# Kernel tuning notes

Hardware: AMD Instinct MI355X
Metric: run time of the kernel (lower is better)

## Reference

```python
import jax, jax.numpy as jnp
import numpy as np

NUM_EXPERTS = 8
HIDDEN = 2048
INTER = 1408
TOKENS = 2048
TOP_K = 2


def setup_inputs() -> dict:
    key = jax.random.key(0)
    k1, k2, k3, k4, k5, k6 = jax.random.split(key, 6)
    hidden_states = jax.random.normal(k1, (TOKENS, HIDDEN), dtype=jnp.float32)
    top_k_index = jax.random.randint(k2, (TOKENS, TOP_K), 0, NUM_EXPERTS)
    top_k_weights = jax.random.uniform(k3, (TOKENS, TOP_K), dtype=jnp.float32)
    top_k_weights = top_k_weights / top_k_weights.sum(-1, keepdims=True)  # router-normalized
    scale = 0.02
    Wg = jax.random.normal(k4, (NUM_EXPERTS, INTER, HIDDEN), dtype=jnp.float32) * scale
    Wu = jax.random.normal(k5, (NUM_EXPERTS, INTER, HIDDEN), dtype=jnp.float32) * scale
    Wd = jax.random.normal(k6, (NUM_EXPERTS, HIDDEN, INTER), dtype=jnp.float32) * scale
    return {
        "hidden_states": hidden_states,
        "top_k_index": top_k_index,
        "top_k_weights": top_k_weights,
        "Wg": Wg,
        "Wu": Wu,
        "Wd": Wd,
    }


def reference(hidden_states, top_k_index, top_k_weights, Wg, Wu, Wd):
    # Combine weight per (token, expert): sum over top-k slots routed to that
    # expert (index_add in the original accumulates duplicate routes identically).
    E = Wg.shape[0]
    cw = (jax.nn.one_hot(top_k_index, E, dtype=hidden_states.dtype)
          * top_k_weights[..., None]).sum(axis=1)            # [T, E]
    # Per-expert SwiGLU MLP computed as grouped GEMMs over all tokens.
    gate = jnp.einsum('th,eih->tei', hidden_states, Wg)       # [T, E, I]
    up = jnp.einsum('th,eih->tei', hidden_states, Wu)         # [T, E, I]
    h = jax.nn.silu(gate) * up                                # [T, E, I]
    out_e = jnp.einsum('tei,ehi->teh', h, Wd)                 # [T, E, H]
    # Weighted combine: tokens not routed to an expert have cw == 0.
    return jnp.einsum('teh,te->th', out_e, cw)                # [T, H]
```

## Files before the change

### kernel.cpp

```cpp
#include <hip/hip_runtime.h>
#include <hip/hip_bf16.h>
#include <stdint.h>

#define TOKENS 2048
#define HIDDEN 2048
#define INTER  1408
#define NEXP   8
#define NPAIR  4096

typedef __attribute__((ext_vector_type(8))) short bf16x8;
typedef __attribute__((ext_vector_type(4))) float f32x4;

static __device__ __forceinline__ unsigned short f2b(float f) {
    union { float f; uint32_t u; } v; v.f = f;
    uint32_t r = (v.u + 0x7FFFu + ((v.u >> 16) & 1u)) >> 16;
    return (unsigned short)r;
}

static __device__ __forceinline__ uint32_t cvtpk(float lo, float hi) {
    uint32_t r;
    asm("v_cvt_pk_bf16_f32 %0, %1, %2" : "=v"(r) : "v"(lo), "v"(hi));
    return r;
}

#define GLDS(SRC, DST) \
    __builtin_amdgcn_global_load_lds( \
        (const __attribute__((address_space(1))) unsigned int*)(SRC), \
        (__attribute__((address_space(3))) unsigned int*)(DST), 16, 0, 0)

__global__ void route_k(const int* __restrict__ idx,
                        int* __restrict__ off, int* __restrict__ tok,
                        int* __restrict__ inv) {
    __shared__ int cnt[NEXP];
    __shared__ int cur[NEXP];
    int tid = threadIdx.x;
    if (tid < NEXP) cnt[tid] = 0;
    __syncthreads();
    for (int i = tid; i < NPAIR; i += 256) atomicAdd(&cnt[idx[i]], 1);
    __syncthreads();
    if (tid == 0) {
        int s = 0;
        for (int e = 0; e < NEXP; ++e) { off[e] = s; cur[e] = s; s += cnt[e]; }
        off[NEXP] = s;
    }
    __syncthreads();
    for (int i = tid; i < NPAIR; i += 256) {
        int e = idx[i];
        int p = atomicAdd(&cur[e], 1);
        tok[p] = i >> 1;
        inv[i] = p;
    }
}

__global__ void conv_k(const float* __restrict__ x, unsigned short* __restrict__ xb, int n) {
    int i = (blockIdx.x * blockDim.x + threadIdx.x) * 4;
    if (i < n) {
        float4 v = *(const float4*)(x + i);
        ushort4 o;
        o.x = f2b(v.x); o.y = f2b(v.y); o.z = f2b(v.z); o.w = f2b(v.w);
        *(ushort4*)(xb + i) = o;
    }
}

__global__ void combine_k(const float* __restrict__ tmp, const int* __restrict__ inv,
                          const float* __restrict__ tw, float* __restrict__ out) {
    int i = blockIdx.x * blockDim.x + threadIdx.x;
    int t = i >> 9;
    int c = (i & 511) * 4;
    int p0 = inv[2 * t], p1 = inv[2 * t + 1];
    float w0 = tw[2 * t], w1 = tw[2 * t + 1];
    float4 x = *(const float4*)(tmp + (size_t)p0 * HIDDEN + c);
    float4 y = *(const float4*)(tmp + (size_t)p1 * HIDDEN + c);
    float4 o;
    o.x = w0 * x.x + w1 * y.x;
    o.y = w0 * x.y + w1 * y.y;
    o.z = w0 * x.z + w1 * y.z;
    o.w = w0 * x.w + w1 * y.w;
    *(float4*)(out + (size_t)t * HIDDEN + c) = o;
}


__global__ __launch_bounds__(256, 4) void gemm1_k(
    const unsigned short* __restrict__ Xb,
    const float* __restrict__ Wg, const float* __restrict__ Wu,
    const int* __restrict__ off, const int* __restrict__ tok,
    unsigned short* __restrict__ H) {

    const int e    = blockIdx.z;
    const int o0   = off[e];
    const int cnt  = off[e + 1] - o0;
    const int row0 = blockIdx.y * 128;
    if (row0 >= cnt) return;
    const int col0 = blockIdx.x * 64;

    __shared__ __align__(16) unsigned short sA[2][128 * 32];
    __shared__ __align__(16) unsigned short sG[2][64 * 32];
    __shared__ __align__(16) unsigned short sU[2][64 * 32];
    __shared__ int stok[128];

    const int tid = threadIdx.x;
    if (tid < 128) {
        int r = row0 + tid;
        stok[tid] = tok[o0 + (r < cnt ? r : cnt - 1)];
    }
    __syncthreads();

    int sa_[2]; const unsigned short* gA[2];
    #pragma unroll
    for (int j = 0; j < 2; ++j) {
        int s = tid + 256 * j, r = s >> 2, q = s & 3;
        sa_[j] = s * 8;
        gA[j] = Xb + (size_t)stok[r] * HIDDEN + ((q ^ ((r >> 1) & 3)) << 3);
    }
    int sb_; const float* fG; const float* fU;
    {
        int s = tid, r = s >> 2, q = s & 3;
        sb_ = s * 8;
        int c = (q ^ ((r >> 1) & 3)) << 3;
        fG = Wg + ((size_t)e * INTER + col0 + r) * HIDDEN + c;
        fU = Wu + ((size_t)e * INTER + col0 + r) * HIDDEN + c;
    }

    const int wave = tid >> 6, lane = tid & 63;
    const int wm = (wave >> 1) * 64, wn = (wave & 1) * 32;
    const int lm = lane & 15, quad = lane >> 4;
    const int swz = ((quad ^ ((lane >> 1) & 3)) << 3);

    f32x4 accg[4][2], accu[4][2];
    #pragma unroll
    for (int i = 0; i < 4; ++i)
        #pragma unroll
        for (int j = 0; j < 2; ++j) {
            accg[i][j] = (f32x4){0.f, 0.f, 0.f, 0.f};
            accu[i][j] = (f32x4){0.f, 0.f, 0.f, 0.f};
        }

    GLDS(gA[0], &sA[0][sa_[0]]);
    GLDS(gA[1], &sA[0][sa_[1]]);
    {
        float4 g0 = *(const float4*)(fG);
        float4 g1 = *(const float4*)(fG + 4);
        float4 u0 = *(const float4*)(fU);
        float4 u1 = *(const float4*)(fU + 4);
        *(int4*)&sG[0][sb_] = make_int4(cvtpk(g0.x, g0.y), cvtpk(g0.z, g0.w),
                                        cvtpk(g1.x, g1.y), cvtpk(g1.z, g1.w));
        *(int4*)&sU[0][sb_] = make_int4(cvtpk(u0.x, u0.y), cvtpk(u0.z, u0.w),
                                        cvtpk(u1.x, u1.y), cvtpk(u1.z, u1.w));
    }
    __syncthreads();

    const int NS = HIDDEN / 32;
    for (int ks = 0; ks < NS; ++ks) {
        const int b = ks & 1;
        float4 g0, g1, u0, u1;
        if (ks + 1 < NS) {
            const int ko = (ks + 1) * 32;
            GLDS(gA[0] + ko, &sA[b ^ 1][sa_[0]]);
            GLDS(gA[1] + ko, &sA[b ^ 1][sa_[1]]);
            g0 = *(const float4*)(fG + ko);
            g1 = *(const float4*)(fG + ko + 4);
            u0 = *(const float4*)(fU + ko);
            u1 = *(const float4*)(fU + ko + 4);
        }
        bf16x8 af[4], gf[2], uf[2];
        #pragma unroll
        for (int mi = 0; mi < 4; ++mi)
            af[mi] = *(const bf16x8*)&sA[b][(wm + mi * 16 + lm) * 32 + swz];
        #pragma unroll
        for (int ni = 0; ni < 2; ++ni) {
            gf[ni] = *(const bf16x8*)&sG[b][(wn + ni * 16 + lm) * 32 + swz];
            uf[ni] = *(const bf16x8*)&sU[b][(wn + ni * 16 + lm) * 32 + swz];
        }
        #pragma unroll
        for (int mi = 0; mi < 4; ++mi)
            #pragma unroll
            for (int ni = 0; ni < 2; ++ni) {
                accg[mi][ni] = __builtin_amdgcn_mfma_f32_16x16x32_bf16(af[mi], gf[ni], accg[mi][ni], 0, 0, 0);
                accu[mi][ni] = __builtin_amdgcn_mfma_f32_16x16x32_bf16(af[mi], uf[ni], accu[mi][ni], 0, 0, 0);
            }
        if (ks + 1 < NS) {
            *(int4*)&sG[b ^ 1][sb_] = make_int4(cvtpk(g0.x, g0.y), cvtpk(g0.z, g0.w),
                                                cvtpk(g1.x, g1.y), cvtpk(g1.z, g1.w));
            *(int4*)&sU[b ^ 1][sb_] = make_int4(cvtpk(u0.x, u0.y), cvtpk(u0.z, u0.w),
                                                cvtpk(u1.x, u1.y), cvtpk(u1.z, u1.w));
        }
        __syncthreads();
    }

    #pragma unroll
    for (int mi = 0; mi < 4; ++mi) {
        #pragma unroll
        for (int reg = 0; reg < 4; ++reg) {
            int lr = wm + mi * 16 + quad * 4 + reg;
            int r  = row0 + lr;
            if (r < cnt) {
                size_t hrow = (size_t)(o0 + r) * INTER;
                #pragma unroll
                for (int ni = 0; ni < 2; ++ni) {
                    float g = accg[mi][ni][reg];
                    float u = accu[mi][ni][reg];
                    float h = g / (1.f + __expf(-g)) * u;
                    H[hrow + col0 + wn + ni * 16 + lm] = f2b(h);
                }
            }
        }
    }
}

__global__ __launch_bounds__(256, 4) void gemm2_k(
    const unsigned short* __restrict__ H,
    const float* __restrict__ Wd,
    const int* __restrict__ off,
    float* __restrict__ tmp) {

    const int e    = blockIdx.z;
    const int o0   = off[e];
    const int cnt  = off[e + 1] - o0;
    const int row0 = blockIdx.y * 128;
    if (row0 >= cnt) return;
    const int col0 = blockIdx.x * 64;

    __shared__ __align__(16) unsigned short sA[2][128 * 32];
    __shared__ __align__(16) unsigned short sB[2][64 * 32];

    const int tid = threadIdx.x;

    int sa_[2]; const unsigned short* gA[2];
    #pragma unroll
    for (int j = 0; j < 2; ++j) {
        int s = tid + 256 * j, r = s >> 2, q = s & 3;
        sa_[j] = s * 8;
        int c = (q ^ ((r >> 1) & 3)) << 3;
        int gr = row0 + r; if (gr >= cnt) gr = cnt - 1;
        gA[j] = H + (size_t)(o0 + gr) * INTER + c;
    }
    int sb_; const float* fB;
    {
        int s = tid, r = s >> 2, q = s & 3;
        sb_ = s * 8;
        int c = (q ^ ((r >> 1) & 3)) << 3;
        fB = Wd + ((size_t)e * HIDDEN + col0 + r) * INTER + c;
    }

    const int wave = tid >> 6, lane = tid & 63;
    const int wm = (wave >> 1) * 64, wn = (wave & 1) * 32;
    const int lm = lane & 15, quad = lane >> 4;
    const int swz = ((quad ^ ((lane >> 1) & 3)) << 3);

    f32x4 acc[4][2];
    #pragma unroll
    for (int i = 0; i < 4; ++i)
        #pragma unroll
        for (int j = 0; j < 2; ++j) acc[i][j] = (f32x4){0.f, 0.f, 0.f, 0.f};

    GLDS(gA[0], &sA[0][sa_[0]]);
    GLDS(gA[1], &sA[0][sa_[1]]);
    {
        float4 b0 = *(const float4*)(fB);
        float4 b1 = *(const float4*)(fB + 4);
        *(int4*)&sB[0][sb_] = make_int4(cvtpk(b0.x, b0.y), cvtpk(b0.z, b0.w),
                                        cvtpk(b1.x, b1.y), cvtpk(b1.z, b1.w));
    }
    __syncthreads();

    const int NS = INTER / 32;
    for (int ks = 0; ks < NS; ++ks) {
        const int b = ks & 1;
        float4 b0, b1;
        if (ks + 1 < NS) {
            const int ko = (ks + 1) * 32;
            GLDS(gA[0] + ko, &sA[b ^ 1][sa_[0]]);
            GLDS(gA[1] + ko, &sA[b ^ 1][sa_[1]]);
            b0 = *(const float4*)(fB + ko);
            b1 = *(const float4*)(fB + ko + 4);
        }
        bf16x8 af[4], bf[2];
        #pragma unroll
        for (int mi = 0; mi < 4; ++mi)
            af[mi] = *(const bf16x8*)&sA[b][(wm + mi * 16 + lm) * 32 + swz];
        #pragma unroll
        for (int ni = 0; ni < 2; ++ni)
            bf[ni] = *(const bf16x8*)&sB[b][(wn + ni * 16 + lm) * 32 + swz];
        #pragma unroll
        for (int mi = 0; mi < 4; ++mi)
            #pragma unroll
            for (int ni = 0; ni < 2; ++ni)
                acc[mi][ni] = __builtin_amdgcn_mfma_f32_16x16x32_bf16(af[mi], bf[ni], acc[mi][ni], 0, 0, 0);
        if (ks + 1 < NS) {
            *(int4*)&sB[b ^ 1][sb_] = make_int4(cvtpk(b0.x, b0.y), cvtpk(b0.z, b0.w),
                                                cvtpk(b1.x, b1.y), cvtpk(b1.z, b1.w));
        }
        __syncthreads();
    }

    #pragma unroll
    for (int mi = 0; mi < 4; ++mi) {
        #pragma unroll
        for (int reg = 0; reg < 4; ++reg) {
            int lr = wm + mi * 16 + quad * 4 + reg;
            int r  = row0 + lr;
            if (r < cnt) {
                size_t trow = (size_t)(o0 + r) * HIDDEN;
                #pragma unroll
                for (int ni = 0; ni < 2; ++ni)
                    tmp[trow + col0 + wn + ni * 16 + lm] = acc[mi][ni][reg];
            }
        }
    }
}

extern "C" void kernel_launch(void* const* d_in, const int* in_sizes, int n_in,
                              void* d_out, int out_size, void* d_ws, size_t ws_size,
                              hipStream_t stream) {
    const float* X   = (const float*)d_in[0];
    const int*   idx = (const int*)d_in[1];
    const float* tw  = (const float*)d_in[2];
    const float* Wg  = (const float*)d_in[3];
    const float* Wu  = (const float*)d_in[4];
    const float* Wd  = (const float*)d_in[5];
    float* out = (float*)d_out;

    char* ws = (char*)d_ws;
    const size_t OFF_TOK = 64;
    const size_t OFF_INV = OFF_TOK + (size_t)NPAIR * 4;
    const size_t OFF_XB  = 65536;
    const size_t OFF_H   = OFF_XB + (size_t)TOKENS * HIDDEN * 2;
    const size_t OFF_TMP = OFF_H + (size_t)NPAIR * INTER * 2;

    int*            off = (int*)ws;
    int*            tok = (int*)(ws + OFF_TOK);
    int*            inv = (int*)(ws + OFF_INV);
    unsigned short* Xb  = (unsigned short*)(ws + OFF_XB);
    unsigned short* H   = (unsigned short*)(ws + OFF_H);
    float*          tmp = (float*)(ws + OFF_TMP);

    route_k<<<1, 256, 0, stream>>>(idx, off, tok, inv);
    conv_k<<<(TOKENS * HIDDEN / 4 + 255) / 256, 256, 0, stream>>>(X, Xb, TOKENS * HIDDEN);

    gemm1_k<<<dim3(INTER / 64, NPAIR / 128, NEXP), 256, 0, stream>>>(Xb, Wg, Wu, off, tok, H);
    gemm2_k<<<dim3(HIDDEN / 64, NPAIR / 128, NEXP), 256, 0, stream>>>(H, Wd, off, tmp);
    combine_k<<<TOKENS * (HIDDEN / 4) / 256, 256, 0, stream>>>(tmp, inv, tw, out);
}
```

Measured before the change: 433.8 us.

## Deepen weight prefetch with register double-buffering and manual vmcnt waits

Both expert GEMM main loops are unrolled by two. The fp32 weight tiles are now loaded two K-steps ahead into alternating register sets, instead of one step ahead. `__syncthreads` is replaced by explicit `s_waitcnt vmcnt(N)` plus `s_barrier`, so the look-ahead weight loads can stay in flight across the barrier while the async A-tile loads to LDS are still guaranteed complete. Scheduling fences keep the compiler from reordering the loads. The aim is to hide global-memory latency on the weight stream, at the cost of extra registers and fragile hand-counted waitcnt values.

```diff
diff --git a/kernel.cpp b/kernel.cpp
--- a/kernel.cpp
+++ b/kernel.cpp
@@ -27,6 +27,10 @@
     __builtin_amdgcn_global_load_lds( \
         (const __attribute__((address_space(1))) unsigned int*)(SRC), \
         (__attribute__((address_space(3))) unsigned int*)(DST), 16, 0, 0)
+
+#define WAITVM(N) asm volatile("s_waitcnt vmcnt(" #N ") lgkmcnt(0)" ::: "memory")
+#define BARRIER() asm volatile("s_barrier" ::: "memory")
+#define SCHED_FENCE() __builtin_amdgcn_sched_barrier(0)
 
 __global__ void route_k(const int* __restrict__ idx,
                         int* __restrict__ off, int* __restrict__ tok,
@@ -80,6 +84,9 @@
 }
 
 
+struct W4 { float4 g0, g1, u0, u1; };
+struct W2 { float4 b0, b1; };
+
 __global__ __launch_bounds__(256, 4) void gemm1_k(
     const unsigned short* __restrict__ Xb,
     const float* __restrict__ Wg, const float* __restrict__ Wu,
@@ -135,8 +142,11 @@
             accu[i][j] = (f32x4){0.f, 0.f, 0.f, 0.f};
         }
 
+    const int NS = HIDDEN / 32;
+
     GLDS(gA[0], &sA[0][sa_[0]]);
     GLDS(gA[1], &sA[0][sa_[1]]);
+    SCHED_FENCE();
     {
         float4 g0 = *(const float4*)(fG);
         float4 g1 = *(const float4*)(fG + 4);
@@ -147,45 +157,63 @@
         *(int4*)&sU[0][sb_] = make_int4(cvtpk(u0.x, u0.y), cvtpk(u0.z, u0.w),
                                         cvtpk(u1.x, u1.y), cvtpk(u1.z, u1.w));
     }
-    __syncthreads();
-
-    const int NS = HIDDEN / 32;
-    for (int ks = 0; ks < NS; ++ks) {
-        const int b = ks & 1;
-        float4 g0, g1, u0, u1;
-        if (ks + 1 < NS) {
-            const int ko = (ks + 1) * 32;
-            GLDS(gA[0] + ko, &sA[b ^ 1][sa_[0]]);
-            GLDS(gA[1] + ko, &sA[b ^ 1][sa_[1]]);
-            g0 = *(const float4*)(fG + ko);
-            g1 = *(const float4*)(fG + ko + 4);
-            u0 = *(const float4*)(fU + ko);
-            u1 = *(const float4*)(fU + ko + 4);
-        }
-        bf16x8 af[4], gf[2], uf[2];
-        #pragma unroll
-        for (int mi = 0; mi < 4; ++mi)
-            af[mi] = *(const bf16x8*)&sA[b][(wm + mi * 16 + lm) * 32 + swz];
-        #pragma unroll
-        for (int ni = 0; ni < 2; ++ni) {
-            gf[ni] = *(const bf16x8*)&sG[b][(wn + ni * 16 + lm) * 32 + swz];
-            uf[ni] = *(const bf16x8*)&sU[b][(wn + ni * 16 + lm) * 32 + swz];
-        }
-        #pragma unroll
-        for (int mi = 0; mi < 4; ++mi)
-            #pragma unroll
-            for (int ni = 0; ni < 2; ++ni) {
-                accg[mi][ni] = __builtin_amdgcn_mfma_f32_16x16x32_bf16(af[mi], gf[ni], accg[mi][ni], 0, 0, 0);
-                accu[mi][ni] = __builtin_amdgcn_mfma_f32_16x16x32_bf16(af[mi], uf[ni], accu[mi][ni], 0, 0, 0);
-            }
-        if (ks + 1 < NS) {
-            *(int4*)&sG[b ^ 1][sb_] = make_int4(cvtpk(g0.x, g0.y), cvtpk(g0.z, g0.w),
-                                                cvtpk(g1.x, g1.y), cvtpk(g1.z, g1.w));
-            *(int4*)&sU[b ^ 1][sb_] = make_int4(cvtpk(u0.x, u0.y), cvtpk(u0.z, u0.w),
-                                                cvtpk(u1.x, u1.y), cvtpk(u1.z, u1.w));
-        }
-        __syncthreads();
-    }
+    W4 wA, wB;
+    wA.g0 = *(const float4*)(fG + 32);
+    wA.g1 = *(const float4*)(fG + 36);
+    wA.u0 = *(const float4*)(fU + 32);
+    wA.u1 = *(const float4*)(fU + 36);
+    SCHED_FENCE();
+    asm volatile("s_waitcnt lgkmcnt(0)" ::: "memory");
+    BARRIER();
+
+#define G1_STEP(KS, WCUR, WNEXT)                                               \
+    {                                                                          \
+        const int b = (KS) & 1;                                                \
+        if ((KS) + 1 < NS) {                                                   \
+            const int ko = ((KS) + 1) * 32;                                    \
+            GLDS(gA[0] + ko, &sA[b ^ 1][sa_[0]]);                              \
+            GLDS(gA[1] + ko, &sA[b ^ 1][sa_[1]]);                              \
+        }                                                                      \
+        SCHED_FENCE();                                                         \
+        if ((KS) + 2 < NS) {                                                   \
+            const int ko2 = ((KS) + 2) * 32;                                   \
+            WNEXT.g0 = *(const float4*)(fG + ko2);                             \
+            WNEXT.g1 = *(const float4*)(fG + ko2 + 4);                         \
+            WNEXT.u0 = *(const float4*)(fU + ko2);                             \
+            WNEXT.u1 = *(const float4*)(fU + ko2 + 4);                         \
+        }                                                                      \
+        SCHED_FENCE();                                                         \
+        bf16x8 af[4], gf[2], uf[2];                                            \
+        _Pragma("unroll")                                                      \
+        for (int mi = 0; mi < 4; ++mi)                                         \
+            af[mi] = *(const bf16x8*)&sA[b][(wm + mi * 16 + lm) * 32 + swz];   \
+        _Pragma("unroll")                                                      \
+        for (int ni = 0; ni < 2; ++ni) {                                       \
+            gf[ni] = *(const bf16x8*)&sG[b][(wn + ni * 16 + lm) * 32 + swz];   \
+            uf[ni] = *(const bf16x8*)&sU[b][(wn + ni * 16 + lm) * 32 + swz];   \
+        }                                                                      \
+        _Pragma("unroll")                                                      \
+        for (int mi = 0; mi < 4; ++mi)                                         \
+            _Pragma("unroll")                                                  \
+            for (int ni = 0; ni < 2; ++ni) {                                   \
+                accg[mi][ni] = __builtin_amdgcn_mfma_f32_16x16x32_bf16(af[mi], gf[ni], accg[mi][ni], 0, 0, 0); \
+                accu[mi][ni] = __builtin_amdgcn_mfma_f32_16x16x32_bf16(af[mi], uf[ni], accu[mi][ni], 0, 0, 0); \
+            }                                                                  \
+        if ((KS) + 1 < NS) {                                                   \
+            *(int4*)&sG[b ^ 1][sb_] = make_int4(cvtpk(WCUR.g0.x, WCUR.g0.y), cvtpk(WCUR.g0.z, WCUR.g0.w), \
+                                                cvtpk(WCUR.g1.x, WCUR.g1.y), cvtpk(WCUR.g1.z, WCUR.g1.w)); \
+            *(int4*)&sU[b ^ 1][sb_] = make_int4(cvtpk(WCUR.u0.x, WCUR.u0.y), cvtpk(WCUR.u0.z, WCUR.u0.w), \
+                                                cvtpk(WCUR.u1.x, WCUR.u1.y), cvtpk(WCUR.u1.z, WCUR.u1.w)); \
+        }                                                                      \
+        if ((KS) + 2 < NS) { WAITVM(4); } else { WAITVM(0); }                  \
+        BARRIER();                                                             \
+    }
+
+    for (int ks = 0; ks < NS; ks += 2) {
+        G1_STEP(ks,     wA, wB);
+        G1_STEP(ks + 1, wB, wA);
+    }
+#undef G1_STEP
 
     #pragma unroll
     for (int mi = 0; mi < 4; ++mi) {
@@ -253,45 +281,64 @@
         #pragma unroll
         for (int j = 0; j < 2; ++j) acc[i][j] = (f32x4){0.f, 0.f, 0.f, 0.f};
 
+    const int NS = INTER / 32;
+
     GLDS(gA[0], &sA[0][sa_[0]]);
     GLDS(gA[1], &sA[0][sa_[1]]);
+    SCHED_FENCE();
     {
         float4 b0 = *(const float4*)(fB);
         float4 b1 = *(const float4*)(fB + 4);
         *(int4*)&sB[0][sb_] = make_int4(cvtpk(b0.x, b0.y), cvtpk(b0.z, b0.w),
                                         cvtpk(b1.x, b1.y), cvtpk(b1.z, b1.w));
     }
-    __syncthreads();
-
-    const int NS = INTER / 32;
-    for (int ks = 0; ks < NS; ++ks) {
-        const int b = ks & 1;
-        float4 b0, b1;
-        if (ks + 1 < NS) {
-            const int ko = (ks + 1) * 32;
-            GLDS(gA[0] + ko, &sA[b ^ 1][sa_[0]]);
-            GLDS(gA[1] + ko, &sA[b ^ 1][sa_[1]]);
-            b0 = *(const float4*)(fB + ko);
-            b1 = *(const float4*)(fB + ko + 4);
-        }
-        bf16x8 af[4], bf[2];
-        #pragma unroll
-        for (int mi = 0; mi < 4; ++mi)
-            af[mi] = *(const bf16x8*)&sA[b][(wm + mi * 16 + lm) * 32 + swz];
-        #pragma unroll
-        for (int ni = 0; ni < 2; ++ni)
-            bf[ni] = *(const bf16x8*)&sB[b][(wn + ni * 16 + lm) * 32 + swz];
-        #pragma unroll
-        for (int mi = 0; mi < 4; ++mi)
-            #pragma unroll
-            for (int ni = 0; ni < 2; ++ni)
-                acc[mi][ni] = __builtin_amdgcn_mfma_f32_16x16x32_bf16(af[mi], bf[ni], acc[mi][ni], 0, 0, 0);
-        if (ks + 1 < NS) {
-            *(int4*)&sB[b ^ 1][sb_] = make_int4(cvtpk(b0.x, b0.y), cvtpk(b0.z, b0.w),
-                                                cvtpk(b1.x, b1.y), cvtpk(b1.z, b1.w));
-        }
-        __syncthreads();
-    }
+    W2 wA, wB;
+    wA.b0 = *(const float4*)(fB + 32);
+    wA.b1 = *(const float4*)(fB + 36);
+    SCHED_FENCE();
+    asm volatile("s_waitcnt lgkmcnt(0)" ::: "memory");
+    BARRIER();
+
+#define G2_STEP(KS, WCUR, WNEXT)                                               \
+    {                                                                          \
+        const int b = (KS) & 1;                                                \
+        if ((KS) + 1 < NS) {                                                   \
+            const int ko = ((KS) + 1) * 32;                                    \
+            GLDS(gA[0] + ko, &sA[b ^ 1][sa_[0]]);                              \
+            GLDS(gA[1] + ko, &sA[b ^ 1][sa_[1]]);                              \
+        }                                                                      \
+        SCHED_FENCE();                                                         \
+        if ((KS) + 2 < NS) {                                                   \
+            const int ko2 = ((KS) + 2) * 32;                                   \
+            WNEXT.b0 = *(const float4*)(fB + ko2);                             \
+            WNEXT.b1 = *(const float4*)(fB + ko2 + 4);                         \
+        }                                                                      \
+        SCHED_FENCE();                                                         \
+        bf16x8 af[4], bfr[2];                                                  \
+        _Pragma("unroll")                                                      \
+        for (int mi = 0; mi < 4; ++mi)                                         \
+            af[mi] = *(const bf16x8*)&sA[b][(wm + mi * 16 + lm) * 32 + swz];   \
+        _Pragma("unroll")                                                      \
+        for (int ni = 0; ni < 2; ++ni)                                         \
+            bfr[ni] = *(const bf16x8*)&sB[b][(wn + ni * 16 + lm) * 32 + swz];  \
+        _Pragma("unroll")                                                      \
+        for (int mi = 0; mi < 4; ++mi)                                         \
+            _Pragma("unroll")                                                  \
+            for (int ni = 0; ni < 2; ++ni)                                     \
+                acc[mi][ni] = __builtin_amdgcn_mfma_f32_16x16x32_bf16(af[mi], bfr[ni], acc[mi][ni], 0, 0, 0); \
+        if ((KS) + 1 < NS) {                                                   \
+            *(int4*)&sB[b ^ 1][sb_] = make_int4(cvtpk(WCUR.b0.x, WCUR.b0.y), cvtpk(WCUR.b0.z, WCUR.b0.w), \
+                                                cvtpk(WCUR.b1.x, WCUR.b1.y), cvtpk(WCUR.b1.z, WCUR.b1.w)); \
+        }                                                                      \
+        if ((KS) + 2 < NS) { WAITVM(2); } else { WAITVM(0); }                  \
+        BARRIER();                                                             \
+    }
+
+    for (int ks = 0; ks < NS; ks += 2) {
+        G2_STEP(ks,     wA, wB);
+        G2_STEP(ks + 1, wB, wA);
+    }
+#undef G2_STEP
 
     #pragma unroll
     for (int mi = 0; mi < 4; ++mi) {
```

Result: slower. 670.6 us (+54.6%).

## Double M-tile to 256 rows with 512-thread blocks in both expert GEMMs

Applied to the files above, without the earlier changes.

Both grouped GEMMs now use 512-thread blocks covering 256 token rows instead of 128, so each fp32 weight tile is loaded from global memory and converted to bf16 half as many times per expert. In gemm1 the gate and up weight loads are split across the two thread halves instead of every thread loading both. The cost is more LDS per block, fewer blocks (and more padded tail rows for experts with small counts), and idle threads during the gemm2 B-tile load.

```diff
diff --git a/kernel.cpp b/kernel.cpp
--- a/kernel.cpp
+++ b/kernel.cpp
@@ -80,7 +80,7 @@
 }
 
 
-__global__ __launch_bounds__(256, 4) void gemm1_k(
+__global__ __launch_bounds__(512, 6) void gemm1_k(
     const unsigned short* __restrict__ Xb,
     const float* __restrict__ Wg, const float* __restrict__ Wu,
     const int* __restrict__ off, const int* __restrict__ tok,
@@ -89,17 +89,17 @@
     const int e    = blockIdx.z;
     const int o0   = off[e];
     const int cnt  = off[e + 1] - o0;
-    const int row0 = blockIdx.y * 128;
+    const int row0 = blockIdx.y * 256;
     if (row0 >= cnt) return;
     const int col0 = blockIdx.x * 64;
 
-    __shared__ __align__(16) unsigned short sA[2][128 * 32];
+    __shared__ __align__(16) unsigned short sA[2][256 * 32];
     __shared__ __align__(16) unsigned short sG[2][64 * 32];
     __shared__ __align__(16) unsigned short sU[2][64 * 32];
-    __shared__ int stok[128];
+    __shared__ int stok[256];
 
     const int tid = threadIdx.x;
-    if (tid < 128) {
+    if (tid < 256) {
         int r = row0 + tid;
         stok[tid] = tok[o0 + (r < cnt ? r : cnt - 1)];
     }
@@ -108,17 +108,22 @@
     int sa_[2]; const unsigned short* gA[2];
     #pragma unroll
     for (int j = 0; j < 2; ++j) {
-        int s = tid + 256 * j, r = s >> 2, q = s & 3;
+        int s = tid + 512 * j, r = s >> 2, q = s & 3;
         sa_[j] = s * 8;
         gA[j] = Xb + (size_t)stok[r] * HIDDEN + ((q ^ ((r >> 1) & 3)) << 3);
     }
-    int sb_; const float* fG; const float* fU;
+    int sb_; const float* fW; unsigned short* sWbase0; unsigned short* sWbase1;
     {
-        int s = tid, r = s >> 2, q = s & 3;
+        int s = tid & 255, r = s >> 2, q = s & 3;
         sb_ = s * 8;
         int c = (q ^ ((r >> 1) & 3)) << 3;
-        fG = Wg + ((size_t)e * INTER + col0 + r) * HIDDEN + c;
-        fU = Wu + ((size_t)e * INTER + col0 + r) * HIDDEN + c;
+        if (tid < 256) {
+            fW = Wg + ((size_t)e * INTER + col0 + r) * HIDDEN + c;
+            sWbase0 = &sG[0][0]; sWbase1 = &sG[1][0];
+        } else {
+            fW = Wu + ((size_t)e * INTER + col0 + r) * HIDDEN + c;
+            sWbase0 = &sU[0][0]; sWbase1 = &sU[1][0];
+        }
     }
 
     const int wave = tid >> 6, lane = tid & 63;
@@ -138,29 +143,23 @@
     GLDS(gA[0], &sA[0][sa_[0]]);
     GLDS(gA[1], &sA[0][sa_[1]]);
     {
-        float4 g0 = *(const float4*)(fG);
-        float4 g1 = *(const float4*)(fG + 4);
-        float4 u0 = *(const float4*)(fU);
-        float4 u1 = *(const float4*)(fU + 4);
-        *(int4*)&sG[0][sb_] = make_int4(cvtpk(g0.x, g0.y), cvtpk(g0.z, g0.w),
-                                        cvtpk(g1.x, g1.y), cvtpk(g1.z, g1.w));
-        *(int4*)&sU[0][sb_] = make_int4(cvtpk(u0.x, u0.y), cvtpk(u0.z, u0.w),
-                                        cvtpk(u1.x, u1.y), cvtpk(u1.z, u1.w));
+        float4 w0 = *(const float4*)(fW);
+        float4 w1 = *(const float4*)(fW + 4);
+        *(int4*)(sWbase0 + sb_) = make_int4(cvtpk(w0.x, w0.y), cvtpk(w0.z, w0.w),
+                                            cvtpk(w1.x, w1.y), cvtpk(w1.z, w1.w));
     }
     __syncthreads();
 
     const int NS = HIDDEN / 32;
     for (int ks = 0; ks < NS; ++ks) {
         const int b = ks & 1;
-        float4 g0, g1, u0, u1;
+        float4 w0, w1;
         if (ks + 1 < NS) {
             const int ko = (ks + 1) * 32;
             GLDS(gA[0] + ko, &sA[b ^ 1][sa_[0]]);
             GLDS(gA[1] + ko, &sA[b ^ 1][sa_[1]]);
-            g0 = *(const float4*)(fG + ko);
-            g1 = *(const float4*)(fG + ko + 4);
-            u0 = *(const float4*)(fU + ko);
-            u1 = *(const float4*)(fU + ko + 4);
+            w0 = *(const float4*)(fW + ko);
+            w1 = *(const float4*)(fW + ko + 4);
         }
         bf16x8 af[4], gf[2], uf[2];
         #pragma unroll
@@ -179,10 +178,9 @@
                 accu[mi][ni] = __builtin_amdgcn_mfma_f32_16x16x32_bf16(af[mi], uf[ni], accu[mi][ni], 0, 0, 0);
             }
         if (ks + 1 < NS) {
-            *(int4*)&sG[b ^ 1][sb_] = make_int4(cvtpk(g0.x, g0.y), cvtpk(g0.z, g0.w),
-                                                cvtpk(g1.x, g1.y), cvtpk(g1.z, g1.w));
-            *(int4*)&sU[b ^ 1][sb_] = make_int4(cvtpk(u0.x, u0.y), cvtpk(u0.z, u0.w),
-                                                cvtpk(u1.x, u1.y), cvtpk(u1.z, u1.w));
+            unsigned short* dst = (b ? sWbase0 : sWbase1);
+            *(int4*)(dst + sb_) = make_int4(cvtpk(w0.x, w0.y), cvtpk(w0.z, w0.w),
+                                            cvtpk(w1.x, w1.y), cvtpk(w1.z, w1.w));
         }
         __syncthreads();
     }
@@ -207,7 +205,7 @@
     }
 }
 
-__global__ __launch_bounds__(256, 4) void gemm2_k(
+__global__ __launch_bounds__(512, 6) void gemm2_k(
     const unsigned short* __restrict__ H,
     const float* __restrict__ Wd,
     const int* __restrict__ off,
@@ -216,11 +214,11 @@
     const int e    = blockIdx.z;
     const int o0   = off[e];
     const int cnt  = off[e + 1] - o0;
-    const int row0 = blockIdx.y * 128;
+    const int row0 = blockIdx.y * 256;
     if (row0 >= cnt) return;
     const int col0 = blockIdx.x * 64;
 
-    __shared__ __align__(16) unsigned short sA[2][128 * 32];
+    __shared__ __align__(16) unsigned short sA[2][256 * 32];
     __shared__ __align__(16) unsigned short sB[2][64 * 32];
 
     const int tid = threadIdx.x;
@@ -228,18 +226,19 @@
     int sa_[2]; const unsigned short* gA[2];
     #pragma unroll
     for (int j = 0; j < 2; ++j) {
-        int s = tid + 256 * j, r = s >> 2, q = s & 3;
+        int s = tid + 512 * j, r = s >> 2, q = s & 3;
         sa_[j] = s * 8;
         int c = (q ^ ((r >> 1) & 3)) << 3;
         int gr = row0 + r; if (gr >= cnt) gr = cnt - 1;
         gA[j] = H + (size_t)(o0 + gr) * INTER + c;
     }
-    int sb_; const float* fB;
+    int sb_; const float* fB = nullptr;
     {
-        int s = tid, r = s >> 2, q = s & 3;
+        int s = tid & 255, r = s >> 2, q = s & 3;
         sb_ = s * 8;
         int c = (q ^ ((r >> 1) & 3)) << 3;
-        fB = Wd + ((size_t)e * HIDDEN + col0 + r) * INTER + c;
+        if (tid < 256)
+            fB = Wd + ((size_t)e * HIDDEN + col0 + r) * INTER + c;
     }
 
     const int wave = tid >> 6, lane = tid & 63;
@@ -255,7 +254,7 @@
 
     GLDS(gA[0], &sA[0][sa_[0]]);
     GLDS(gA[1], &sA[0][sa_[1]]);
-    {
+    if (tid < 256) {
         float4 b0 = *(const float4*)(fB);
         float4 b1 = *(const float4*)(fB + 4);
         *(int4*)&sB[0][sb_] = make_int4(cvtpk(b0.x, b0.y), cvtpk(b0.z, b0.w),
@@ -271,22 +270,24 @@
             const int ko = (ks + 1) * 32;
             GLDS(gA[0] + ko, &sA[b ^ 1][sa_[0]]);
             GLDS(gA[1] + ko, &sA[b ^ 1][sa_[1]]);
-            b0 = *(const float4*)(fB + ko);
-            b1 = *(const float4*)(fB + ko + 4);
-        }
-        bf16x8 af[4], bf[2];
+            if (tid < 256) {
+                b0 = *(const float4*)(fB + ko);
+                b1 = *(const float4*)(fB + ko + 4);
+            }
+        }
+        bf16x8 af[4], bfr[2];
         #pragma unroll
         for (int mi = 0; mi < 4; ++mi)
             af[mi] = *(const bf16x8*)&sA[b][(wm + mi * 16 + lm) * 32 + swz];
         #pragma unroll
         for (int ni = 0; ni < 2; ++ni)
-            bf[ni] = *(const bf16x8*)&sB[b][(wn + ni * 16 + lm) * 32 + swz];
+            bfr[ni] = *(const bf16x8*)&sB[b][(wn + ni * 16 + lm) * 32 + swz];
         #pragma unroll
         for (int mi = 0; mi < 4; ++mi)
             #pragma unroll
             for (int ni = 0; ni < 2; ++ni)
-                acc[mi][ni] = __builtin_amdgcn_mfma_f32_16x16x32_bf16(af[mi], bf[ni], acc[mi][ni], 0, 0, 0);
-        if (ks + 1 < NS) {
+                acc[mi][ni] = __builtin_amdgcn_mfma_f32_16x16x32_bf16(af[mi], bfr[ni], acc[mi][ni], 0, 0, 0);
+        if (ks + 1 < NS && tid < 256) {
             *(int4*)&sB[b ^ 1][sb_] = make_int4(cvtpk(b0.x, b0.y), cvtpk(b0.z, b0.w),
                                                 cvtpk(b1.x, b1.y), cvtpk(b1.z, b1.w));
         }
@@ -337,7 +338,7 @@
     route_k<<<1, 256, 0, stream>>>(idx, off, tok, inv);
     conv_k<<<(TOKENS * HIDDEN / 4 + 255) / 256, 256, 0, stream>>>(X, Xb, TOKENS * HIDDEN);
 
-    gemm1_k<<<dim3(INTER / 64, NPAIR / 128, NEXP), 256, 0, stream>>>(Xb, Wg, Wu, off, tok, H);
-    gemm2_k<<<dim3(HIDDEN / 64, NPAIR / 128, NEXP), 256, 0, stream>>>(H, Wd, off, tmp);
+    gemm1_k<<<dim3(INTER / 64, NPAIR / 256, NEXP), 512, 0, stream>>>(Xb, Wg, Wu, off, tok, H);
+    gemm2_k<<<dim3(HIDDEN / 64, NPAIR / 256, NEXP), 512, 0, stream>>>(H, Wd, off, tmp);
     combine_k<<<TOKENS * (HIDDEN / 4) / 256, 256, 0, stream>>>(tmp, inv, tw, out);
 }
```

Result: slower. 859.0 us (+98.0%).
